# Optimization experiments

Hardware: AMD Instinct MI355X
Metric: run time of the kernel (lower is better)

## Reference

```python
import jax, jax.numpy as jnp
import numpy as np

N, D = 512, 64          # n_objects, object_dim
HG, OG = 256, 256       # g hidden, g output
HF, OF = 256, 64        # f hidden, f output


def setup_inputs() -> dict:
    key = jax.random.key(0)
    ks = jax.random.split(key, 16)
    s = 0.05
    inp = {
        "x": jax.random.normal(ks[0], (N, D), dtype=jnp.float32),
        "q": jax.random.normal(ks[1], (D,), dtype=jnp.float32),
        # MLP g: input 3*D -> HG -> OG (ReLU after every layer, nonlinear=True)
        "g_w1": jax.random.normal(ks[2], (3 * D, HG), dtype=jnp.float32) * s,
        "g_b1": jnp.zeros((HG,), dtype=jnp.float32),
        "g_w2": jax.random.normal(ks[3], (HG, OG), dtype=jnp.float32) * s,
        "g_b2": jnp.zeros((OG,), dtype=jnp.float32),
        # query_expand: D -> HG -> OG (nonlinear=True)
        "qe_w1": jax.random.normal(ks[4], (D, HG), dtype=jnp.float32) * s,
        "qe_b1": jnp.zeros((HG,), dtype=jnp.float32),
        "qe_w2": jax.random.normal(ks[5], (HG, OG), dtype=jnp.float32) * s,
        "qe_b2": jnp.zeros((OG,), dtype=jnp.float32),
        # MLP f: OG -> HF -> OF (ReLU on hidden only, nonlinear=False)
        "f_w1": jax.random.normal(ks[6], (OG, HF), dtype=jnp.float32) * s,
        "f_b1": jnp.zeros((HF,), dtype=jnp.float32),
        "f_w2": jax.random.normal(ks[7], (HF, OF), dtype=jnp.float32) * s,
        "f_b2": jnp.zeros((OF,), dtype=jnp.float32),
    }
    return inp


def reference(x, q, g_w1, g_b1, g_w2, g_b2, qe_w1, qe_b1, qe_w2, qe_b2,
              f_w1, f_b1, f_w2, f_b2):
    n, d = x.shape
    # pair (a,b): first half x_i = x[b], second half x_j = x[a], then query q
    xi = jnp.broadcast_to(x[None, :, :], (n, n, d))   # repeats x along dim 0
    xj = jnp.broadcast_to(x[:, None, :], (n, n, d))   # repeats x along dim 1
    qb = jnp.broadcast_to(q[None, None, :], (n, n, d))
    pair_concat = jnp.concatenate([xi, xj, qb], axis=-1).reshape(n * n, 3 * d)
    # g MLP (ReLU after every layer since nonlinear=True)
    h = jax.nn.relu(pair_concat @ g_w1 + g_b1)
    relations = jax.nn.relu(h @ g_w2 + g_b2)          # [N*N, OG]
    # attentional weighting
    qh = jax.nn.relu(q @ qe_w1 + qe_b1)
    q_exp = jax.nn.relu(qh @ qe_w2 + qe_b2)           # [OG]
    c = jax.nn.softmax(relations @ q_exp, axis=0)     # [N*N]
    embedding = jnp.sum(relations * c[:, None], axis=0)  # [OG]
    # f MLP (no final nonlinearity)
    fh = jax.nn.relu(embedding @ f_w1 + f_b1)
    out = fh @ f_w2 + f_b2                            # [OF]
    return out
```

## Files before the change

kernel.cpp:

```cpp
#include <hip/hip_runtime.h>
#include <hip/hip_bf16.h>

typedef __attribute__((ext_vector_type(8))) short s16x8;
typedef __attribute__((ext_vector_type(4))) float f32x4;

#define NSLOT 128

__device__ __forceinline__ short f2bf(float f) {
    union { float f; unsigned u; } c; c.f = f;
    unsigned u = c.u;
    return (short)((u + 0x7fffu + ((u >> 16) & 1u)) >> 16);
}

__global__ __launch_bounds__(256) void rn_k1(
    const float* __restrict__ x, const float* __restrict__ q,
    const float* __restrict__ g_w1, const float* __restrict__ g_b1,
    const float* __restrict__ g_w2,
    const float* __restrict__ qe_w1, const float* __restrict__ qe_b1,
    const float* __restrict__ qe_w2, const float* __restrict__ qe_b2,
    float* __restrict__ U, float* __restrict__ V,
    float* __restrict__ c0, float* __restrict__ qexp,
    short* __restrict__ w2s, float* __restrict__ accb)
{
    __shared__ float sbuf[64];
    __shared__ float qh[256];
    const int blk = blockIdx.x, t = threadIdx.x;

    if (blk < 512) {
        if (t < 64) sbuf[t] = x[blk * 64 + t];
        __syncthreads();
        float u = 0.f, v = 0.f;
        #pragma unroll 4
        for (int k = 0; k < 64; ++k) {
            float xv = sbuf[k];
            u += xv * g_w1[k * 256 + t];
            v += xv * g_w1[(64 + k) * 256 + t];
        }
        U[blk * 256 + t] = u;
        V[blk * 256 + t] = v;
        {
            int E = blk * 256 + t;
            int e = E & 7, f = E >> 3;
            int lane = f & 63, n = (f >> 6) & 3, kk = (f >> 8) & 7, wv = (f >> 11) & 3;
            int l15 = lane & 15, g = lane >> 4;
            int col = wv * 64 + n * 16 + l15;
            int k = kk * 32 + g * 8 + e;
            w2s[E] = f2bf(g_w2[k * 256 + col]);
        }
    } else if (blk == 512) {
        if (t < 64) sbuf[t] = q[t];
        __syncthreads();
        float cc = g_b1[t], hh = qe_b1[t];
        #pragma unroll 4
        for (int k = 0; k < 64; ++k) {
            float qv = sbuf[k];
            cc += qv * g_w1[(128 + k) * 256 + t];
            hh += qv * qe_w1[k * 256 + t];
        }
        c0[t] = cc;
        qh[t] = fmaxf(hh, 0.f);
        __syncthreads();
        float qe = qe_b2[t];
        #pragma unroll 4
        for (int k = 0; k < 256; ++k) qe += qh[k] * qe_w2[k * 256 + t];
        qexp[t] = fmaxf(qe, 0.f);
    } else {
        const int total = NSLOT * 257;
        int off = (blk - 513) * 2048 + t * 8;
        #pragma unroll
        for (int i = 0; i < 8; ++i)
            if (off + i < total) accb[off + i] = 0.f;
    }
}

__global__ __launch_bounds__(256, 4) void rn_k2(
    const float* __restrict__ U, const float* __restrict__ V,
    const float* __restrict__ c0, const float* __restrict__ qexp,
    const short* __restrict__ w2s, const float* __restrict__ g_b2,
    float* __restrict__ accb)
{
    __shared__ short hT[64][264];
    __shared__ float srowT[64][4];

    const int bid = blockIdx.x;
    const int a   = bid >> 3;
    const int b0  = (bid & 7) << 6;
    const int tid = threadIdx.x;
    const int wave = tid >> 6, lane = tid & 63;
    const int l15 = lane & 15, g = lane >> 4;
    const int col0 = wave << 6;

    {
        const int c4 = tid & 63;
        const int r0 = tid >> 6;
        const float4 vv  = *(const float4*)&V[a * 256 + c4 * 4];
        const float4 cc  = *(const float4*)&c0[c4 * 4];
        const float4 vcv = make_float4(vv.x + cc.x, vv.y + cc.y,
                                       vv.z + cc.z, vv.w + cc.w);
        #pragma unroll
        for (int it = 0; it < 16; ++it) {
            int row = r0 + it * 4;
            float4 uu = *(const float4*)&U[(b0 + row) * 256 + c4 * 4];
            __hip_bfloat162 p0 = __float22bfloat162_rn(
                make_float2(fmaxf(uu.x + vcv.x, 0.f), fmaxf(uu.y + vcv.y, 0.f)));
            __hip_bfloat162 p1 = __float22bfloat162_rn(
                make_float2(fmaxf(uu.z + vcv.z, 0.f), fmaxf(uu.w + vcv.w, 0.f)));
            uint2 st;
            st.x = *reinterpret_cast<unsigned*>(&p0);
            st.y = *reinterpret_cast<unsigned*>(&p1);
            *reinterpret_cast<uint2*>(&hT[row][c4 * 4]) = st;
        }
    }

    float qe[4], b2c[4];
    #pragma unroll
    for (int n = 0; n < 4; ++n) {
        int col = col0 + n * 16 + l15;
        qe[n]  = qexp[col];
        b2c[n] = g_b2[col];
    }
    __syncthreads();

    f32x4 acc[4][4];
    #pragma unroll
    for (int m = 0; m < 4; ++m)
        #pragma unroll
        for (int n = 0; n < 4; ++n)
            acc[m][n] = (f32x4){0.f, 0.f, 0.f, 0.f};

    #pragma unroll
    for (int kk = 0; kk < 8; ++kk) {
        const int koff = kk * 32 + g * 8;
        s16x8 bfr[4];
        #pragma unroll
        for (int n = 0; n < 4; ++n)
            bfr[n] = *(const s16x8*)&w2s[(((wave * 8 + kk) * 4 + n) * 64 + lane) * 8];
        s16x8 afr[4];
        #pragma unroll
        for (int m = 0; m < 4; ++m)
            afr[m] = *(const s16x8*)&hT[m * 16 + l15][koff];
        #pragma unroll
        for (int m = 0; m < 4; ++m)
            #pragma unroll
            for (int n = 0; n < 4; ++n)
                acc[m][n] = __builtin_amdgcn_mfma_f32_16x16x32_bf16(
                    afr[m], bfr[n], acc[m][n], 0, 0, 0);
    }

    #pragma unroll
    for (int m = 0; m < 4; ++m)
        #pragma unroll
        for (int n = 0; n < 4; ++n)
            #pragma unroll
            for (int j = 0; j < 4; ++j)
                acc[m][n][j] = fmaxf(acc[m][n][j] + b2c[n], 0.f);

    #pragma unroll
    for (int m = 0; m < 4; ++m) {
        #pragma unroll
        for (int j = 0; j < 4; ++j) {
            float sp = 0.f;
            #pragma unroll
            for (int n = 0; n < 4; ++n) sp += acc[m][n][j] * qe[n];
            sp += __shfl_xor(sp, 1);
            sp += __shfl_xor(sp, 2);
            sp += __shfl_xor(sp, 4);
            sp += __shfl_xor(sp, 8);
            if (l15 == 0) srowT[m * 16 + g * 4 + j][wave] = sp;
        }
    }
    __syncthreads();

    float wrow[4][4];
    #pragma unroll
    for (int m = 0; m < 4; ++m)
        #pragma unroll
        for (int j = 0; j < 4; ++j) {
            const float4 s4 = *(const float4*)&srowT[m * 16 + g * 4 + j][0];
            wrow[m][j] = __expf(s4.x + s4.y + s4.z + s4.w);
        }

    const int slot = bid & (NSLOT - 1);
    if (wave == 0) {
        float ls = 0.f;
        #pragma unroll
        for (int m = 0; m < 4; ++m)
            #pragma unroll
            for (int j = 0; j < 4; ++j) ls += wrow[m][j];
        ls += __shfl_xor(ls, 16);
        ls += __shfl_xor(ls, 32);
        if (lane == 0) atomicAdd(&accb[slot * 257 + 256], ls);
    }

    #pragma unroll
    for (int n = 0; n < 4; ++n) {
        float wv = 0.f;
        #pragma unroll
        for (int m = 0; m < 4; ++m)
            #pragma unroll
            for (int j = 0; j < 4; ++j)
                wv += wrow[m][j] * acc[m][n][j];
        wv += __shfl_xor(wv, 16);
        wv += __shfl_xor(wv, 32);
        if (lane < 16) atomicAdd(&accb[slot * 257 + col0 + n * 16 + lane], wv);
    }
}

__global__ __launch_bounds__(256) void rn_k4(
    const float* __restrict__ accb,
    const float* __restrict__ f_w1, const float* __restrict__ f_b1,
    const float* __restrict__ f_w2, const float* __restrict__ f_b2,
    float* __restrict__ out)
{
    __shared__ float emb[256];
    __shared__ float fh[256];
    const int t = threadIdx.x;

    float v = 0.f, ls = 0.f;
    #pragma unroll 8
    for (int s = 0; s < NSLOT; ++s) {
        v  += accb[s * 257 + t];
        ls += accb[s * 257 + 256];
    }
    emb[t] = v / ls;
    __syncthreads();

    float h = f_b1[t];
    #pragma unroll 4
    for (int k = 0; k < 256; ++k) h += emb[k] * f_w1[k * 256 + t];
    fh[t] = fmaxf(h, 0.f);
    __syncthreads();

    if (t < 64) {
        float o = f_b2[t];
        #pragma unroll 4
        for (int k = 0; k < 256; ++k) o += fh[k] * f_w2[k * 64 + t];
        out[t] = o;
    }
}

extern "C" void kernel_launch(void* const* d_in, const int* in_sizes, int n_in,
                              void* d_out, int out_size, void* d_ws, size_t ws_size,
                              hipStream_t stream) {
    const float* x     = (const float*)d_in[0];
    const float* q     = (const float*)d_in[1];
    const float* g_w1  = (const float*)d_in[2];
    const float* g_b1  = (const float*)d_in[3];
    const float* g_w2  = (const float*)d_in[4];
    const float* g_b2  = (const float*)d_in[5];
    const float* qe_w1 = (const float*)d_in[6];
    const float* qe_b1 = (const float*)d_in[7];
    const float* qe_w2 = (const float*)d_in[8];
    const float* qe_b2 = (const float*)d_in[9];
    const float* f_w1  = (const float*)d_in[10];
    const float* f_b1  = (const float*)d_in[11];
    const float* f_w2  = (const float*)d_in[12];
    const float* f_b2  = (const float*)d_in[13];

    float* wsf  = (float*)d_ws;
    float* U    = wsf;
    float* V    = wsf + 131072;
    float* c0   = wsf + 262144;
    float* qexp = wsf + 262400;
    short* w2s  = (short*)(wsf + 262656);
    float* accb = wsf + 328192;

    hipLaunchKernelGGL(rn_k1, dim3(530), dim3(256), 0, stream,
                       x, q, g_w1, g_b1, g_w2, qe_w1, qe_b1, qe_w2, qe_b2,
                       U, V, c0, qexp, w2s, accb);
    hipLaunchKernelGGL(rn_k2, dim3(4096), dim3(256), 0, stream,
                       U, V, c0, qexp, (const short*)w2s, g_b2, accb);
    hipLaunchKernelGGL(rn_k4, dim3(1), dim3(256), 0, stream,
                       accb, f_w1, f_b1, f_w2, f_b2, (float*)d_out);
}
```

Baseline: 83.06 us.

## Restructure prep and tail kernels: register-tiled U/V, coalesced w2 swizzle, 1024-thread f-MLP

The prep kernel now computes U/V with 64 blocks. Each block caches 16 rows of x in shared memory and holds a column of g_w1 in registers, replacing 512 blocks that each reread the weights. The bf16 swizzle of g_w2 becomes a separate set of blocks that read g_w2 with coalesced float4 loads and scatter the writes. The main kernel folds the g_b2 bias into the accumulator initialisation and simplifies its index arithmetic. The single-block tail kernel uses 1024 threads to split the slot reduction and both f-MLP layers four ways, which shortens the serial dependency chains at the cost of extra shared-memory partial sums and barriers.

```diff
diff --git a/kernel.cpp b/kernel.cpp
--- a/kernel.cpp
+++ b/kernel.cpp
@@ -22,32 +22,39 @@
     float* __restrict__ c0, float* __restrict__ qexp,
     short* __restrict__ w2s, float* __restrict__ accb)
 {
-    __shared__ float sbuf[64];
-    __shared__ float qh[256];
     const int blk = blockIdx.x, t = threadIdx.x;
 
-    if (blk < 512) {
-        if (t < 64) sbuf[t] = x[blk * 64 + t];
+    if (blk < 64) {
+        __shared__ float xs[1024];
+        const int rg = blk >> 1, half = blk & 1;
+        const int r0 = rg << 4;
+        #pragma unroll
+        for (int i = 0; i < 4; ++i) {
+            int idx = i * 256 + t;
+            xs[idx] = x[(r0 << 6) + idx];
+        }
+        float w[64];
+        #pragma unroll
+        for (int k = 0; k < 64; ++k)
+            w[k] = g_w1[(half * 64 + k) * 256 + t];
         __syncthreads();
-        float u = 0.f, v = 0.f;
-        #pragma unroll 4
-        for (int k = 0; k < 64; ++k) {
-            float xv = sbuf[k];
-            u += xv * g_w1[k * 256 + t];
-            v += xv * g_w1[(64 + k) * 256 + t];
-        }
-        U[blk * 256 + t] = u;
-        V[blk * 256 + t] = v;
-        {
-            int E = blk * 256 + t;
-            int e = E & 7, f = E >> 3;
-            int lane = f & 63, n = (f >> 6) & 3, kk = (f >> 8) & 7, wv = (f >> 11) & 3;
-            int l15 = lane & 15, g = lane >> 4;
-            int col = wv * 64 + n * 16 + l15;
-            int k = kk * 32 + g * 8 + e;
-            w2s[E] = f2bf(g_w2[k * 256 + col]);
-        }
-    } else if (blk == 512) {
+        float* dst = half ? V : U;
+        #pragma unroll 2
+        for (int r = 0; r < 16; ++r) {
+            float a0 = 0.f, a1 = 0.f, a2 = 0.f, a3 = 0.f;
+            #pragma unroll
+            for (int k = 0; k < 64; k += 4) {
+                const float4 xv = *(const float4*)&xs[r * 64 + k];
+                a0 += xv.x * w[k + 0];
+                a1 += xv.y * w[k + 1];
+                a2 += xv.z * w[k + 2];
+                a3 += xv.w * w[k + 3];
+            }
+            dst[(r0 + r) * 256 + t] = (a0 + a1) + (a2 + a3);
+        }
+    } else if (blk == 64) {
+        __shared__ float sbuf[64];
+        __shared__ float qh[256];
         if (t < 64) sbuf[t] = q[t];
         __syncthreads();
         float cc = g_b1[t], hh = qe_b1[t];
@@ -64,9 +71,23 @@
         #pragma unroll 4
         for (int k = 0; k < 256; ++k) qe += qh[k] * qe_w2[k * 256 + t];
         qexp[t] = fmaxf(qe, 0.f);
+    } else if (blk < 97) {
+        const int S0 = (blk - 65) * 2048 + t * 8;
+        const float4 wA = *(const float4*)&g_w2[S0];
+        const float4 wB = *(const float4*)&g_w2[S0 + 4];
+        float wv8[8] = {wA.x, wA.y, wA.z, wA.w, wB.x, wB.y, wB.z, wB.w};
+        #pragma unroll
+        for (int i = 0; i < 8; ++i) {
+            const int S = S0 + i;
+            const int k = S >> 8, col = S & 255;
+            const int wv = col >> 6, n = (col >> 4) & 3, l15 = col & 15;
+            const int kk = k >> 5, g = (k >> 3) & 3, e = k & 7;
+            const int lane = g * 16 + l15;
+            w2s[((((wv * 8 + kk) * 4 + n) * 64 + lane) << 3) + e] = f2bf(wv8[i]);
+        }
     } else {
         const int total = NSLOT * 257;
-        int off = (blk - 513) * 2048 + t * 8;
+        int off = (blk - 97) * 2048 + t * 8;
         #pragma unroll
         for (int i = 0; i < 8; ++i)
             if (off + i < total) accb[off + i] = 0.f;
@@ -126,7 +147,7 @@
     for (int m = 0; m < 4; ++m)
         #pragma unroll
         for (int n = 0; n < 4; ++n)
-            acc[m][n] = (f32x4){0.f, 0.f, 0.f, 0.f};
+            acc[m][n] = (f32x4){b2c[n], b2c[n], b2c[n], b2c[n]};
 
     #pragma unroll
     for (int kk = 0; kk < 8; ++kk) {
@@ -134,7 +155,7 @@
         s16x8 bfr[4];
         #pragma unroll
         for (int n = 0; n < 4; ++n)
-            bfr[n] = *(const s16x8*)&w2s[(((wave * 8 + kk) * 4 + n) * 64 + lane) * 8];
+            bfr[n] = *(const s16x8*)&w2s[((wave << 14) + (((kk * 4 + n) << 9))) + (lane << 3)];
         s16x8 afr[4];
         #pragma unroll
         for (int m = 0; m < 4; ++m)
@@ -153,7 +174,7 @@
         for (int n = 0; n < 4; ++n)
             #pragma unroll
             for (int j = 0; j < 4; ++j)
-                acc[m][n][j] = fmaxf(acc[m][n][j] + b2c[n], 0.f);
+                acc[m][n][j] = fmaxf(acc[m][n][j], 0.f);
 
     #pragma unroll
     for (int m = 0; m < 4; ++m) {
@@ -206,37 +227,61 @@
     }
 }
 
-__global__ __launch_bounds__(256) void rn_k4(
+__global__ __launch_bounds__(1024) void rn_k4(
     const float* __restrict__ accb,
     const float* __restrict__ f_w1, const float* __restrict__ f_b1,
     const float* __restrict__ f_w2, const float* __restrict__ f_b2,
     float* __restrict__ out)
 {
+    __shared__ float part[4][256];
     __shared__ float emb[256];
     __shared__ float fh[256];
-    const int t = threadIdx.x;
-
-    float v = 0.f, ls = 0.f;
+    __shared__ float lsa[128];
+    const int t   = threadIdx.x;
+    const int col = t & 255;
+    const int sl  = t >> 8;
+
+    float v = 0.f;
     #pragma unroll 8
-    for (int s = 0; s < NSLOT; ++s) {
-        v  += accb[s * 257 + t];
-        ls += accb[s * 257 + 256];
-    }
-    emb[t] = v / ls;
-    __syncthreads();
-
-    float h = f_b1[t];
-    #pragma unroll 4
-    for (int k = 0; k < 256; ++k) h += emb[k] * f_w1[k * 256 + t];
-    fh[t] = fmaxf(h, 0.f);
-    __syncthreads();
-
-    if (t < 64) {
-        float o = f_b2[t];
-        #pragma unroll 4
-        for (int k = 0; k < 256; ++k) o += fh[k] * f_w2[k * 64 + t];
-        out[t] = o;
-    }
+    for (int s = sl; s < NSLOT; s += 4) v += accb[s * 257 + col];
+    part[sl][col] = v;
+    if (t < 128) lsa[t] = accb[t * 257 + 256];
+    __syncthreads();
+
+    if (sl == 0) {
+        float ls = 0.f;
+        #pragma unroll 8
+        for (int s = 0; s < 128; ++s) ls += lsa[s];
+        emb[col] = (part[0][col] + part[1][col] + part[2][col] + part[3][col]) / ls;
+    }
+    __syncthreads();
+
+    {
+        float h = 0.f;
+        const int k0 = sl << 6;
+        #pragma unroll 8
+        for (int k = 0; k < 64; ++k)
+            h += emb[k0 + k] * f_w1[(k0 + k) * 256 + col];
+        part[sl][col] = h;
+    }
+    __syncthreads();
+    if (sl == 0)
+        fh[col] = fmaxf(part[0][col] + part[1][col] + part[2][col] + part[3][col]
+                        + f_b1[col], 0.f);
+    __syncthreads();
+
+    if (t < 256) {
+        const int oc = t & 63, ks = t >> 6;
+        float o = 0.f;
+        const int k0 = ks << 6;
+        #pragma unroll 8
+        for (int k = 0; k < 64; ++k)
+            o += fh[k0 + k] * f_w2[(k0 + k) * 64 + oc];
+        part[ks][oc] = o;
+    }
+    __syncthreads();
+    if (t < 64)
+        out[t] = part[0][t] + part[1][t] + part[2][t] + part[3][t] + f_b2[t];
 }
 
 extern "C" void kernel_launch(void* const* d_in, const int* in_sizes, int n_in,
@@ -263,13 +308,13 @@
     float* c0   = wsf + 262144;
     float* qexp = wsf + 262400;
     short* w2s  = (short*)(wsf + 262656);
-    float* accb = wsf + 328192;
-
-    hipLaunchKernelGGL(rn_k1, dim3(530), dim3(256), 0, stream,
+    float* accb = wsf + 295424;
+
+    hipLaunchKernelGGL(rn_k1, dim3(114), dim3(256), 0, stream,
                        x, q, g_w1, g_b1, g_w2, qe_w1, qe_b1, qe_w2, qe_b2,
                        U, V, c0, qexp, w2s, accb);
     hipLaunchKernelGGL(rn_k2, dim3(4096), dim3(256), 0, stream,
                        U, V, c0, qexp, (const short*)w2s, g_b2, accb);
-    hipLaunchKernelGGL(rn_k4, dim3(1), dim3(256), 0, stream,
+    hipLaunchKernelGGL(rn_k4, dim3(1), dim3(1024), 0, stream,
                        accb, f_w1, f_b1, f_w2, f_b2, (float*)d_out);
 }
```

Result: faster. 72.59 us (-12.6%).
